# Performance work log

Hardware: AMD Instinct MI355X
Metric: run time of the kernel (lower is better)

The kernel has to match this reference:

```python
import jax, jax.numpy as jnp
import numpy as np

DIM = 512
DIM_HEAD = 32
HEADS = DIM // DIM_HEAD
WS = 8  # window (partition) size
INNER = (DIM * 4 * 2 // 3 // 32) * 32  # gated-MLP inner dim = 2720
EPS = 1e-6
LS_INIT = 1e-5


def _ln(x, g, b):
    mu = jnp.mean(x, axis=-1, keepdims=True)
    var = jnp.var(x, axis=-1, keepdims=True)
    return (x - mu) * jax.lax.rsqrt(var + EPS) * g + b


def setup_inputs() -> dict:
    key = jax.random.key(0)
    ks = jax.random.split(key, 8)
    B, H, W = 8, 96, 96
    s = lambda d: 1.0 / np.sqrt(d)
    return {
        "x": jax.random.normal(ks[0], (B, H, W, DIM), jnp.float32),
        "norm1_g": jnp.ones((DIM,), jnp.float32),
        "norm1_b": jnp.zeros((DIM,), jnp.float32),
        "qkv_w": jax.random.normal(ks[1], (DIM, 3 * DIM), jnp.float32) * s(DIM),
        "qkv_b": jnp.zeros((3 * DIM,), jnp.float32),
        "proj_w": jax.random.normal(ks[2], (DIM, DIM), jnp.float32) * s(DIM),
        "proj_b": jnp.zeros((DIM,), jnp.float32),
        "ls1": jnp.full((DIM,), LS_INIT, jnp.float32),
        "norm2_g": jnp.ones((DIM,), jnp.float32),
        "norm2_b": jnp.zeros((DIM,), jnp.float32),
        "glu_w": jax.random.normal(ks[3], (DIM, 2 * INNER), jnp.float32) * s(DIM),
        "glu_b": jnp.zeros((2 * INNER,), jnp.float32),
        "fc2_w": jax.random.normal(ks[4], (INNER, DIM), jnp.float32) * s(INNER),
        "fc2_b": jnp.zeros((DIM,), jnp.float32),
        "ls2": jnp.full((DIM,), LS_INIT, jnp.float32),
    }


def reference(x, norm1_g, norm1_b, qkv_w, qkv_b, proj_w, proj_b, ls1,
              norm2_g, norm2_b, glu_w, glu_b, fc2_w, fc2_b, ls2):
    B, H, W, C = x.shape
    nH, nW = H // WS, W // WS
    T = WS * WS  # tokens per window

    # ---- window attention branch ----
    y = _ln(x, norm1_g, norm1_b)
    # window_partition: (B,H,W,C) -> (B*nH*nW, T, C)
    y = y.reshape(B, nH, WS, nW, WS, C).transpose(0, 1, 3, 2, 4, 5)
    y = y.reshape(-1, T, C)
    qkv = y @ qkv_w + qkv_b                      # (M, T, 3C)
    qkv = qkv.reshape(-1, T, 3, HEADS, DIM_HEAD)
    q, k, v = qkv[:, :, 0], qkv[:, :, 1], qkv[:, :, 2]   # (M, T, h, d)
    scale = DIM_HEAD ** -0.5
    attn = jnp.einsum('mqhd,mkhd->mhqk', q, k) * scale
    attn = jax.nn.softmax(attn, axis=-1)
    o = jnp.einsum('mhqk,mkhd->mqhd', attn, v).reshape(-1, T, C)
    o = o @ proj_w + proj_b
    # window_reverse: (M, T, C) -> (B, H, W, C)
    o = o.reshape(B, nH, nW, WS, WS, C).transpose(0, 1, 3, 2, 4, 5)
    o = o.reshape(B, H, W, C)
    x = x + ls1 * o

    # ---- gated MLP branch (GLU with SiLU) ----
    y = _ln(x, norm2_g, norm2_b)
    h = y @ glu_w + glu_b
    h, gate = jnp.split(h, 2, axis=-1)
    h = h * jax.nn.silu(gate)
    h = h @ fc2_w + fc2_b
    x = x + ls2 * h
    return x
```

## Files before the change

kernel.cpp:

```cpp
#include <hip/hip_runtime.h>
#include <hip/hip_bf16.h>
#include <stdint.h>

#define DIM 512
#define HEADS 16
#define NTOK 73728
#define INNER 1344
#define INNERP 1408

typedef __attribute__((ext_vector_type(8))) short vbf8;
typedef __attribute__((ext_vector_type(4))) float vf4;
typedef __attribute__((ext_vector_type(4))) int v4i;
typedef __attribute__((ext_vector_type(8))) int v8i;

typedef __attribute__((address_space(1))) void as1void;
typedef __attribute__((address_space(3))) void as3void;

__device__ __forceinline__ unsigned pk4fp8(float a, float b, float c, float d) {
  int v = __builtin_amdgcn_cvt_pk_fp8_f32(a, b, 0, false);
  v = __builtin_amdgcn_cvt_pk_fp8_f32(c, d, v, true);
  return (unsigned)v;
}

__global__ void k_transpose(const float* __restrict__ Wsrc, uint8_t* __restrict__ WT,
                            int K, int N, int ldOut, int nsplit) {
  __shared__ float tile[32][33];
  const int tx = threadIdx.x, ty = threadIdx.y;
  const int n0 = blockIdx.x * 32, k0 = blockIdx.y * 32;
#pragma unroll
  for (int i = 0; i < 32; i += 8) {
    int k = k0 + ty + i, n = n0 + tx;
    if (k < K && n < N) tile[ty + i][tx] = Wsrc[(size_t)k * N + n];
  }
  __syncthreads();
#pragma unroll
  for (int i = 0; i < 32; i += 8) {
    int n = n0 + ty + i, k = k0 + tx;
    if (n < N && k < K) {
      int np = n + (n >= nsplit ? 64 : 0);
      float v = tile[tx][ty + i];
      WT[(size_t)np * ldOut + k] =
          (uint8_t)(__builtin_amdgcn_cvt_pk_fp8_f32(v, v, 0, false) & 0xff);
    }
  }
}

__global__ void k_padbias(const float* __restrict__ b, float* __restrict__ o) {
  int c = blockIdx.x * 256 + threadIdx.x;
  if (c < INNER) o[c] = b[c];
  else if (c >= INNERP && c < INNERP + INNER) o[c] = b[c - 64];
  else if (c < 2816) o[c] = 0.0f;
}

template <bool PART>
__global__ __launch_bounds__(256) void k_ln(const float* __restrict__ x,
                                            const float* __restrict__ gw,
                                            const float* __restrict__ bw,
                                            uint8_t* __restrict__ y) {
  const int wave = threadIdx.x >> 6, lane = threadIdx.x & 63;
  const int tok = blockIdx.x * 4 + wave;
  const float* xr = x + (size_t)tok * DIM + lane * 8;
  const float4 v0 = *(const float4*)xr;
  const float4 v1 = *(const float4*)(xr + 4);
  float s = v0.x + v0.y + v0.z + v0.w + v1.x + v1.y + v1.z + v1.w;
  float ss = v0.x * v0.x + v0.y * v0.y + v0.z * v0.z + v0.w * v0.w +
             v1.x * v1.x + v1.y * v1.y + v1.z * v1.z + v1.w * v1.w;
#pragma unroll
  for (int off = 32; off > 0; off >>= 1) {
    s += __shfl_xor(s, off);
    ss += __shfl_xor(ss, off);
  }
  const float mu = s * (1.0f / DIM);
  const float rs = rsqrtf(ss * (1.0f / DIM) - mu * mu + 1e-6f);
  size_t orow;
  if (PART) {
    int b = tok / 9216, rem = tok % 9216;
    int h = rem / 96, w = rem % 96;
    orow = (size_t)(((b * 12 + (h >> 3)) * 12 + (w >> 3)) * 64 + (h & 7) * 8 + (w & 7));
  } else {
    orow = (size_t)tok;
  }
  const float4 g0 = *(const float4*)(gw + lane * 8);
  const float4 g1 = *(const float4*)(gw + lane * 8 + 4);
  const float4 b0 = *(const float4*)(bw + lane * 8);
  const float4 b1 = *(const float4*)(bw + lane * 8 + 4);
  const float vals[8] = {v0.x, v0.y, v0.z, v0.w, v1.x, v1.y, v1.z, v1.w};
  const float gg[8] = {g0.x, g0.y, g0.z, g0.w, g1.x, g1.y, g1.z, g1.w};
  const float bb[8] = {b0.x, b0.y, b0.z, b0.w, b1.x, b1.y, b1.z, b1.w};
  float r[8];
#pragma unroll
  for (int j = 0; j < 8; ++j) r[j] = (vals[j] - mu) * rs * gg[j] + bb[j];
  uint2 po;
  po.x = pk4fp8(r[0], r[1], r[2], r[3]);
  po.y = pk4fp8(r[4], r[5], r[6], r[7]);
  *(uint2*)(y + orow * DIM + lane * 8) = po;
}

template <int ROWS>
__device__ __forceinline__ void stage_lds8(const uint8_t* __restrict__ g, int ldKb,
                                           char* lds, int wave, int lane) {
  constexpr int RPW = ROWS / 4;
  const int r0 = wave * RPW;
  const int ro = lane >> 3;
  const int pb = lane & 7;
  const uint8_t* src = g + (size_t)(r0 + ro) * (size_t)ldKb + ((pb ^ ro) << 4);
  char* dst = lds + r0 * 128;
#pragma unroll
  for (int c = 0; c < RPW; c += 8) {
    __builtin_amdgcn_global_load_lds((const as1void*)(src + (size_t)c * (size_t)ldKb),
                                     (as3void*)(dst + c * 128), 16, 0, 0);
  }
}

__device__ __forceinline__ v8i lds_frag8(const char* base, int row, int g) {
  const int ro = row & 7;
  const v4i lo = *(const v4i*)(base + row * 128 + (((2 * g) ^ ro) << 4));
  const v4i hi = *(const v4i*)(base + row * 128 + (((2 * g + 1) ^ ro) << 4));
  return __builtin_shufflevector(lo, hi, 0, 1, 2, 3, 4, 5, 6, 7);
}

#define MFMA_SC(a, b, c) \
  __builtin_amdgcn_mfma_scale_f32_16x16x128_f8f6f4((a), (b), (c), 0, 0, 0, 127, 0, 127)

template <int MODE, int NT>
__global__ __launch_bounds__(256, 2) void k_gemm128(const uint8_t* __restrict__ A,
                                                    const uint8_t* __restrict__ BT,
                                                    const float* __restrict__ bias,
                                                    void* __restrict__ outp,
                                                    const float* __restrict__ resid,
                                                    const float* __restrict__ lsv, int K,
                                                    int ldOut) {
  __shared__ alignas(16) char As[128 * 128];
  __shared__ alignas(16) char Bs[128 * 128];
  const int nwg = gridDim.x;
  int bid = blockIdx.x;
  bid = (bid & 7) * (nwg >> 3) + (bid >> 3);
  const int bm = bid / NT, bn = bid % NT;
  const int tid = threadIdx.x;
  const int wave = tid >> 6, lane = tid & 63;
  const int wr = wave >> 1, wc = wave & 1;
  vf4 acc[4][4] = {};

  const uint8_t* Ab = A + (size_t)bm * 128 * K;
  const uint8_t* Bb = BT + (size_t)bn * 128 * K;
  const int cl = lane & 15, g = lane >> 4;
  const int arow = wr * 64 + cl;
  const int brow = wc * 64 + cl;
  const int nkt = K >> 7;

  for (int t = 0; t < nkt; ++t) {
    __syncthreads();
    stage_lds8<128>(Ab + t * 128, K, As, wave, lane);
    stage_lds8<128>(Bb + t * 128, K, Bs, wave, lane);
    __syncthreads();
    v8i af[4], bfr[4];
#pragma unroll
    for (int i = 0; i < 4; ++i) {
      af[i] = lds_frag8(As, arow + i * 16, g);
      bfr[i] = lds_frag8(Bs, brow + i * 16, g);
    }
#pragma unroll
    for (int mi = 0; mi < 4; ++mi)
#pragma unroll
      for (int ni = 0; ni < 4; ++ni)
        acc[mi][ni] = MFMA_SC(af[mi], bfr[ni], acc[mi][ni]);
  }

  const int rl = g << 2;
  const int rbase = bm * 128 + wr * 64;
  const int cbase = bn * 128 + wc * 64;
#pragma unroll
  for (int mi = 0; mi < 4; ++mi) {
#pragma unroll
    for (int j = 0; j < 4; ++j) {
      const int r = rbase + mi * 16 + rl + j;
      size_t orow;
      if (MODE == 1) {
        int m = r >> 6, t = r & 63;
        int b = m / 144, mm = m % 144;
        int wh = mm / 12, ww = mm % 12;
        int h = wh * 8 + (t >> 3), w = ww * 8 + (t & 7);
        orow = (size_t)((b * 96 + h) * 96 + w);
      } else {
        orow = (size_t)r;
      }
#pragma unroll
      for (int ni = 0; ni < 4; ++ni) {
        const int c = cbase + ni * 16 + cl;
        const float v = acc[mi][ni][j] + bias[c];
        if (MODE == 0) {
          ((__hip_bfloat16*)outp)[(size_t)r * ldOut + c] = __float2bfloat16(v);
        } else {
          float* of = (float*)outp;
          of[orow * DIM + c] = resid[orow * DIM + c] + lsv[c] * v;
        }
      }
    }
  }
}

__global__ __launch_bounds__(256, 2) void k_gemm_glu(const uint8_t* __restrict__ A,
                                                     const uint8_t* __restrict__ BT,
                                                     const float* __restrict__ bias,
                                                     uint8_t* __restrict__ hout) {
  __shared__ alignas(16) char As[128 * 128];
  __shared__ alignas(16) char B0s[64 * 128];
  __shared__ alignas(16) char B1s[64 * 128];
  const int K = DIM;
  const int nwg = gridDim.x;
  int bid = blockIdx.x;
  bid = (bid & 7) * (nwg >> 3) + (bid >> 3);
  const int bm = bid / 22, bn = bid % 22;
  const int tid = threadIdx.x;
  const int wave = tid >> 6, lane = tid & 63;
  const int wr = wave >> 1, wc = wave & 1;
  vf4 a0[4][2] = {}, a1[4][2] = {};

  const uint8_t* Ab = A + (size_t)bm * 128 * K;
  const uint8_t* Bb0 = BT + (size_t)(bn * 64) * K;
  const uint8_t* Bb1 = BT + (size_t)(INNERP + bn * 64) * K;
  const int cl = lane & 15, g = lane >> 4;
  const int arow = wr * 64 + cl;
  const int brow = wc * 32 + cl;

#pragma unroll
  for (int t = 0; t < 4; ++t) {
    __syncthreads();
    stage_lds8<128>(Ab + t * 128, K, As, wave, lane);
    stage_lds8<64>(Bb0 + t * 128, K, B0s, wave, lane);
    stage_lds8<64>(Bb1 + t * 128, K, B1s, wave, lane);
    __syncthreads();
    v8i af[4], b0f[2], b1f[2];
#pragma unroll
    for (int i = 0; i < 4; ++i) af[i] = lds_frag8(As, arow + i * 16, g);
#pragma unroll
    for (int i = 0; i < 2; ++i) {
      b0f[i] = lds_frag8(B0s, brow + i * 16, g);
      b1f[i] = lds_frag8(B1s, brow + i * 16, g);
    }
#pragma unroll
    for (int mi = 0; mi < 4; ++mi)
#pragma unroll
      for (int ni = 0; ni < 2; ++ni) {
        a0[mi][ni] = MFMA_SC(af[mi], b0f[ni], a0[mi][ni]);
        a1[mi][ni] = MFMA_SC(af[mi], b1f[ni], a1[mi][ni]);
      }
  }

  const int rl = g << 2;
  const int rbase = bm * 128 + wr * 64;
  const int cbase = bn * 64 + wc * 32;
#pragma unroll
  for (int mi = 0; mi < 4; ++mi)
#pragma unroll
    for (int j = 0; j < 4; ++j) {
      const int r = rbase + mi * 16 + rl + j;
#pragma unroll
      for (int ni = 0; ni < 2; ++ni) {
        const int c = cbase + ni * 16 + cl;
        const float a = a0[mi][ni][j] + bias[c];
        const float gv = a1[mi][ni][j] + bias[INNERP + c];
        const float sg = 1.0f / (1.0f + __expf(-gv));
        const float hv = a * gv * sg;
        hout[(size_t)r * INNERP + c] =
            (uint8_t)(__builtin_amdgcn_cvt_pk_fp8_f32(hv, hv, 0, false) & 0xff);
      }
    }
}

__global__ __launch_bounds__(256, 2) void k_attn_mfma(const __hip_bfloat16* __restrict__ qkv,
                                                      uint8_t* __restrict__ o) {
  __shared__ __hip_bfloat16 sm[4][6912];
  const int wave = threadIdx.x >> 6, lane = threadIdx.x & 63;
  const int task = blockIdx.x * 4 + wave;
  const int w = task >> 4, hd = task & 15;
  const int g = lane >> 4, c = lane & 15;
  __hip_bfloat16* smp = sm[wave];
  __hip_bfloat16* smv = smp + 4608;

  const __hip_bfloat16* base = qkv + (size_t)w * 64 * 1536 + hd * 32;

  vbf8 qf[4], kf[4];
#pragma unroll
  for (int i = 0; i < 4; ++i) {
    const __hip_bfloat16* qrow = base + (size_t)(i * 16 + c) * 1536 + g * 8;
    qf[i] = *(const vbf8*)qrow;
    kf[i] = *(const vbf8*)(qrow + 512);
  }

  {
    const __hip_bfloat16* vrow = base + (size_t)lane * 1536 + 1024;
    union {
      vbf8 v;
      ushort e[8];
    } uv[4];
#pragma unroll
    for (int i = 0; i < 4; ++i) uv[i].v = *(const vbf8*)(vrow + i * 8);
#pragma unroll
    for (int d = 0; d < 32; ++d)
      ((ushort*)smv)[d * 72 + lane] = uv[d >> 3].e[d & 7];
// ... 39 lines not shown
    for (int j = 0; j < 4; ++j) {
      const int q = iq * 16 + g * 4 + j;
#pragma unroll
      for (int it = 0; it < 4; ++it)
        smp[q * 72 + it * 16 + c] = __float2bfloat16(st[iq][it][j]);
    }

  vf4 ot[4][2] = {};
#pragma unroll
  for (int ks = 0; ks < 2; ++ks) {
    vbf8 pf[4], vfr[2];
#pragma unroll
    for (int iq = 0; iq < 4; ++iq)
      pf[iq] = *(const vbf8*)(smp + (iq * 16 + c) * 72 + ks * 32 + g * 8);
#pragma unroll
    for (int dt = 0; dt < 2; ++dt)
      vfr[dt] = *(const vbf8*)(smv + (dt * 16 + c) * 72 + ks * 32 + g * 8);
#pragma unroll
    for (int iq = 0; iq < 4; ++iq)
#pragma unroll
      for (int dt = 0; dt < 2; ++dt)
        ot[iq][dt] = __builtin_amdgcn_mfma_f32_16x16x32_bf16(pf[iq], vfr[dt], ot[iq][dt], 0, 0, 0);
  }

#pragma unroll
  for (int iq = 0; iq < 4; ++iq)
#pragma unroll
    for (int dt = 0; dt < 2; ++dt)
#pragma unroll
      for (int j = 0; j < 4; ++j) {
        const int q = iq * 16 + g * 4 + j;
        smp[q * 72 + dt * 16 + c] = __float2bfloat16(ot[iq][dt][j] * inv[iq][j]);
      }
  uint8_t* ob = o + (size_t)w * 64 * 512 + hd * 32;
#pragma unroll
  for (int i = 0; i < 4; ++i) {
    const int idx = i * 64 + lane;
    const int row = idx >> 2, chunk = idx & 3;
    union {
      vbf8 v;
      ushort e[8];
    } u;
    u.v = *(const vbf8*)(smp + row * 72 + chunk * 8);
    float f[8];
#pragma unroll
    for (int j = 0; j < 8; ++j) f[j] = __uint_as_float((unsigned)u.e[j] << 16);
    uint2 pv;
    pv.x = pk4fp8(f[0], f[1], f[2], f[3]);
    pv.y = pk4fp8(f[4], f[5], f[6], f[7]);
    *(uint2*)(ob + (size_t)row * 512 + chunk * 8) = pv;
  }
}

extern "C" void kernel_launch(void* const* d_in, const int* in_sizes, int n_in, void* d_out,
                              int out_size, void* d_ws, size_t ws_size, hipStream_t stream) {
  const float* x = (const float*)d_in[0];
  const float* n1g = (const float*)d_in[1];
  const float* n1b = (const float*)d_in[2];
  const float* qkv_w = (const float*)d_in[3];
  const float* qkv_b = (const float*)d_in[4];
  const float* proj_w = (const float*)d_in[5];
  const float* proj_b = (const float*)d_in[6];
  const float* ls1 = (const float*)d_in[7];
  const float* n2g = (const float*)d_in[8];
  const float* n2b = (const float*)d_in[9];
  const float* glu_w = (const float*)d_in[10];
  const float* glu_b = (const float*)d_in[11];
  const float* fc2_w = (const float*)d_in[12];
  const float* fc2_b = (const float*)d_in[13];
  const float* ls2 = (const float*)d_in[14];

  if (ws_size < 268000000u) return;

  char* ws = (char*)d_ws;
  uint8_t* wTq = (uint8_t*)(ws + 0);
  uint8_t* wTp = (uint8_t*)(ws + 786432);
  uint8_t* wTg = (uint8_t*)(ws + 1048576);
  uint8_t* wTf = (uint8_t*)(ws + 2490368);
  float* gbias = (float*)(ws + 3211264);
  uint8_t* ybuf = (uint8_t*)(ws + 3222528);
  __hip_bfloat16* qkvbuf = (__hip_bfloat16*)(ws + 40971264);
  uint8_t* hbuf = (uint8_t*)(ws + 40971264);
  float* x1 = (float*)d_out;

  hipMemsetAsync(wTg, 0, 1441792, stream);
  hipMemsetAsync(wTf, 0, 720896, stream);

  dim3 tb(32, 8);
  k_transpose<<<dim3(48, 16), tb, 0, stream>>>(qkv_w, wTq, 512, 1536, 512, 1 << 30);
  k_transpose<<<dim3(16, 16), tb, 0, stream>>>(proj_w, wTp, 512, 512, 512, 1 << 30);
  k_transpose<<<dim3(84, 16), tb, 0, stream>>>(glu_w, wTg, 512, 2688, 512, INNER);
  k_transpose<<<dim3(16, 42), tb, 0, stream>>>(fc2_w, wTf, 1344, 512, 1408, 1 << 30);
  k_padbias<<<11, 256, 0, stream>>>(glu_b, gbias);

  k_ln<true><<<18432, 256, 0, stream>>>(x, n1g, n1b, ybuf);
  k_gemm128<0, 12><<<6912, 256, 0, stream>>>(ybuf, wTq, qkv_b, qkvbuf, nullptr, nullptr, 512, 1536);
  k_attn_mfma<<<4608, 256, 0, stream>>>(qkvbuf, ybuf);
  k_gemm128<1, 4><<<2304, 256, 0, stream>>>(ybuf, wTp, proj_b, (void*)x1, x, ls1, 512, 512);
  k_ln<false><<<18432, 256, 0, stream>>>(x1, n2g, n2b, ybuf);
  k_gemm_glu<<<12672, 256, 0, stream>>>(ybuf, wTg, gbias, hbuf);
  k_gemm128<2, 4><<<2304, 256, 0, stream>>>(hbuf, wTf, fc2_b, d_out, x1, ls2, INNERP, 512);
}
```

Measured before the change: 577.9 us.

## Switch GEMM operands to FP4 with per-32 block weight scales

All activations and weights move from FP8 to FP4 (e2m1). Weights get per-32-element power-of-two block scales, and the GEMMs use the scaled MFMA in fp4 mode with half-size LDS tiles and occupancy raised to 3. The intermediate residual x1 is stored as bf16 instead of fp32, and the GLU epilogue stages results through LDS so it can write packed nibbles. This halves operand bandwidth and LDS traffic, at a large accuracy cost: activations are quantized to FP4 with no scale, which risks exceeding tolerance.

```diff
diff --git a/kernel.cpp b/kernel.cpp
--- a/kernel.cpp
+++ b/kernel.cpp
@@ -1,10 +1,9 @@
 #include <hip/hip_runtime.h>
 #include <hip/hip_bf16.h>
 #include <stdint.h>
+#include <math.h>
 
 #define DIM 512
-#define HEADS 16
-#define NTOK 73728
 #define INNER 1344
 #define INNERP 1408
 
@@ -16,14 +15,31 @@
 typedef __attribute__((address_space(1))) void as1void;
 typedef __attribute__((address_space(3))) void as3void;
 
-__device__ __forceinline__ unsigned pk4fp8(float a, float b, float c, float d) {
-  int v = __builtin_amdgcn_cvt_pk_fp8_f32(a, b, 0, false);
-  v = __builtin_amdgcn_cvt_pk_fp8_f32(c, d, v, true);
-  return (unsigned)v;
-}
-
-__global__ void k_transpose(const float* __restrict__ Wsrc, uint8_t* __restrict__ WT,
-                            int K, int N, int ldOut, int nsplit) {
+union frag8 {
+  v8i w;
+  v4i h[2];
+};
+
+__device__ __forceinline__ uint32_t quant4(float v) {
+  uint32_t s = (__float_as_uint(v) >> 31) << 3;
+  float a = fabsf(v);
+  uint32_t m = (a > 0.25f) + (a > 0.75f) + (a > 1.25f) + (a > 1.75f) +
+               (a > 2.5f) + (a > 3.5f) + (a > 5.0f);
+  return s | m;
+}
+__device__ __forceinline__ uint32_t pack8fp4(const float* r) {
+  uint32_t u = 0;
+#pragma unroll
+  for (int j = 0; j < 8; ++j) u |= quant4(r[j]) << (4 * j);
+  return u;
+}
+
+#define MFMA4(a, b, c, sb) \
+  __builtin_amdgcn_mfma_scale_f32_16x16x128_f8f6f4((a), (b), (c), 4, 4, 0, 127, 0, (sb))
+
+__global__ void k_transpose4(const float* __restrict__ Wsrc, uint8_t* __restrict__ WT,
+                             uint8_t* __restrict__ Wsc, int K, int N, int ldB, int ldS,
+                             int nsplit) {
   __shared__ float tile[32][33];
   const int tx = threadIdx.x, ty = threadIdx.y;
   const int n0 = blockIdx.x * 32, k0 = blockIdx.y * 32;
@@ -33,14 +49,32 @@
     if (k < K && n < N) tile[ty + i][tx] = Wsrc[(size_t)k * N + n];
   }
   __syncthreads();
-#pragma unroll
-  for (int i = 0; i < 32; i += 8) {
-    int n = n0 + ty + i, k = k0 + tx;
-    if (n < N && k < K) {
+  if (tx < 16) {
+#pragma unroll
+    for (int i = 0; i < 32; i += 8) {
+      int n = n0 + ty + i;
+      if (n >= N) continue;
+      float v0 = tile[2 * tx][ty + i], v1 = tile[2 * tx + 1][ty + i];
+      float m = fmaxf(fabsf(v0), fabsf(v1));
+      m = fmaxf(m, __shfl_xor(m, 1));
+      m = fmaxf(m, __shfl_xor(m, 2));
+      m = fmaxf(m, __shfl_xor(m, 4));
+      m = fmaxf(m, __shfl_xor(m, 8));
+      uint8_t sbyte;
+      float s;
+      if (m < 1e-20f) {
+        sbyte = 0;
+        s = 0.0f;
+      } else {
+        int e = (int)ceilf(log2f(m * 0.166666672f));
+        e = e < -126 ? -126 : (e > 126 ? 126 : e);
+        sbyte = (uint8_t)(e + 127);
+        s = exp2f((float)(-e));
+      }
       int np = n + (n >= nsplit ? 64 : 0);
-      float v = tile[tx][ty + i];
-      WT[(size_t)np * ldOut + k] =
-          (uint8_t)(__builtin_amdgcn_cvt_pk_fp8_f32(v, v, 0, false) & 0xff);
+      WT[(size_t)np * ldB + (k0 >> 1) + tx] =
+          (uint8_t)(quant4(v0 * s) | (quant4(v1 * s) << 4));
+      if (tx == 0) Wsc[(size_t)np * ldS + (k0 >> 5)] = sbyte;
     }
   }
 }
@@ -52,19 +86,36 @@
   else if (c < 2816) o[c] = 0.0f;
 }
 
-template <bool PART>
-__global__ __launch_bounds__(256) void k_ln(const float* __restrict__ x,
+template <bool PART, bool BF16IN>
+__global__ __launch_bounds__(256) void k_ln(const void* __restrict__ xin,
                                             const float* __restrict__ gw,
                                             const float* __restrict__ bw,
                                             uint8_t* __restrict__ y) {
   const int wave = threadIdx.x >> 6, lane = threadIdx.x & 63;
   const int tok = blockIdx.x * 4 + wave;
-  const float* xr = x + (size_t)tok * DIM + lane * 8;
-  const float4 v0 = *(const float4*)xr;
-  const float4 v1 = *(const float4*)(xr + 4);
-  float s = v0.x + v0.y + v0.z + v0.w + v1.x + v1.y + v1.z + v1.w;
-  float ss = v0.x * v0.x + v0.y * v0.y + v0.z * v0.z + v0.w * v0.w +
-             v1.x * v1.x + v1.y * v1.y + v1.z * v1.z + v1.w * v1.w;
+  float vals[8];
+  if (BF16IN) {
+    const __hip_bfloat16* xr = (const __hip_bfloat16*)xin + (size_t)tok * DIM + lane * 8;
+    union {
+      vbf8 v;
+      ushort e[8];
+    } u;
+    u.v = *(const vbf8*)xr;
+#pragma unroll
+    for (int j = 0; j < 8; ++j) vals[j] = __uint_as_float((unsigned)u.e[j] << 16);
+  } else {
+    const float* xr = (const float*)xin + (size_t)tok * DIM + lane * 8;
+    const float4 v0 = *(const float4*)xr;
+    const float4 v1 = *(const float4*)(xr + 4);
+    vals[0] = v0.x; vals[1] = v0.y; vals[2] = v0.z; vals[3] = v0.w;
+    vals[4] = v1.x; vals[5] = v1.y; vals[6] = v1.z; vals[7] = v1.w;
+  }
+  float s = 0.f, ss = 0.f;
+#pragma unroll
+  for (int j = 0; j < 8; ++j) {
+    s += vals[j];
+    ss += vals[j] * vals[j];
+  }
 #pragma unroll
   for (int off = 32; off > 0; off >>= 1) {
     s += __shfl_xor(s, off);
@@ -84,86 +135,88 @@
   const float4 g1 = *(const float4*)(gw + lane * 8 + 4);
   const float4 b0 = *(const float4*)(bw + lane * 8);
   const float4 b1 = *(const float4*)(bw + lane * 8 + 4);
-  const float vals[8] = {v0.x, v0.y, v0.z, v0.w, v1.x, v1.y, v1.z, v1.w};
   const float gg[8] = {g0.x, g0.y, g0.z, g0.w, g1.x, g1.y, g1.z, g1.w};
   const float bb[8] = {b0.x, b0.y, b0.z, b0.w, b1.x, b1.y, b1.z, b1.w};
   float r[8];
 #pragma unroll
   for (int j = 0; j < 8; ++j) r[j] = (vals[j] - mu) * rs * gg[j] + bb[j];
-  uint2 po;
-  po.x = pk4fp8(r[0], r[1], r[2], r[3]);
-  po.y = pk4fp8(r[4], r[5], r[6], r[7]);
-  *(uint2*)(y + orow * DIM + lane * 8) = po;
+  *(uint32_t*)(y + orow * 256 + lane * 4) = pack8fp4(r);
 }
 
 template <int ROWS>
-__device__ __forceinline__ void stage_lds8(const uint8_t* __restrict__ g, int ldKb,
-                                           char* lds, int wave, int lane) {
+__device__ __forceinline__ void stage4(const uint8_t* __restrict__ gsrc, int RB, char* lds,
+                                       int wave, int lane) {
   constexpr int RPW = ROWS / 4;
   const int r0 = wave * RPW;
-  const int ro = lane >> 3;
-  const int pb = lane & 7;
-  const uint8_t* src = g + (size_t)(r0 + ro) * (size_t)ldKb + ((pb ^ ro) << 4);
-  char* dst = lds + r0 * 128;
-#pragma unroll
-  for (int c = 0; c < RPW; c += 8) {
-    __builtin_amdgcn_global_load_lds((const as1void*)(src + (size_t)c * (size_t)ldKb),
-                                     (as3void*)(dst + c * 128), 16, 0, 0);
-  }
-}
-
-__device__ __forceinline__ v8i lds_frag8(const char* base, int row, int g) {
-  const int ro = row & 7;
-  const v4i lo = *(const v4i*)(base + row * 128 + (((2 * g) ^ ro) << 4));
-  const v4i hi = *(const v4i*)(base + row * 128 + (((2 * g + 1) ^ ro) << 4));
-  return __builtin_shufflevector(lo, hi, 0, 1, 2, 3, 4, 5, 6, 7);
-}
-
-#define MFMA_SC(a, b, c) \
-  __builtin_amdgcn_mfma_scale_f32_16x16x128_f8f6f4((a), (b), (c), 0, 0, 0, 127, 0, 127)
+  const int srw = lane >> 2, sbk = lane & 3;
+  const uint8_t* src = gsrc + (size_t)(r0 + srw) * RB + ((sbk ^ (srw & 3)) << 4);
+  char* dst = lds + r0 * 64;
+#pragma unroll
+  for (int c = 0; c < RPW; c += 16)
+    __builtin_amdgcn_global_load_lds((const as1void*)(src + (size_t)c * RB),
+                                     (as3void*)(dst + c * 64), 16, 0, 0);
+}
 
 template <int MODE, int NT>
-__global__ __launch_bounds__(256, 2) void k_gemm128(const uint8_t* __restrict__ A,
-                                                    const uint8_t* __restrict__ BT,
-                                                    const float* __restrict__ bias,
-                                                    void* __restrict__ outp,
-                                                    const float* __restrict__ resid,
-                                                    const float* __restrict__ lsv, int K,
-                                                    int ldOut) {
-  __shared__ alignas(16) char As[128 * 128];
-  __shared__ alignas(16) char Bs[128 * 128];
+__global__ __launch_bounds__(256, 3) void k_gemm4(const uint8_t* __restrict__ A4,
+                                                  const uint8_t* __restrict__ B4,
+                                                  const uint8_t* __restrict__ Bsc,
+                                                  const float* __restrict__ bias,
+                                                  void* __restrict__ outp,
+                                                  const void* __restrict__ resid,
+                                                  const float* __restrict__ lsv, const int K,
+                                                  const int ldOut) {
+  __shared__ alignas(16) char As[128 * 64];
+  __shared__ alignas(16) char Bs[128 * 64];
   const int nwg = gridDim.x;
   int bid = blockIdx.x;
   bid = (bid & 7) * (nwg >> 3) + (bid >> 3);
   const int bm = bid / NT, bn = bid % NT;
-  const int tid = threadIdx.x;
-  const int wave = tid >> 6, lane = tid & 63;
+  const int tid = threadIdx.x, wave = tid >> 6, lane = tid & 63;
   const int wr = wave >> 1, wc = wave & 1;
+  const int cl = lane & 15, g = lane >> 4;
+  const int RB = K >> 1, KB = K >> 5, nkt = K >> 7;
+
+  const uint8_t* Ab = A4 + (size_t)bm * 128 * RB;
+  const uint8_t* Bb = B4 + (size_t)bn * 128 * RB;
+
+  int aoff[4], boff[4];
+  const uint8_t* bscp[4];
+#pragma unroll
+  for (int i = 0; i < 4; ++i) {
+    int ra = wr * 64 + cl + i * 16;
+    int rb = wc * 64 + cl + i * 16;
+    aoff[i] = ra * 64 + ((g ^ (ra & 3)) << 4);
+    boff[i] = rb * 64 + ((g ^ (rb & 3)) << 4);
+    bscp[i] = Bsc + (size_t)(bn * 128 + rb) * KB + g;
+  }
+
+  frag8 afr[4], bfr[4];
+#pragma unroll
+  for (int i = 0; i < 4; ++i) {
+    afr[i].w = (v8i){0, 0, 0, 0, 0, 0, 0, 0};
+    bfr[i].w = (v8i){0, 0, 0, 0, 0, 0, 0, 0};
+  }
   vf4 acc[4][4] = {};
-
-  const uint8_t* Ab = A + (size_t)bm * 128 * K;
-  const uint8_t* Bb = BT + (size_t)bn * 128 * K;
-  const int cl = lane & 15, g = lane >> 4;
-  const int arow = wr * 64 + cl;
-  const int brow = wc * 64 + cl;
-  const int nkt = K >> 7;
 
   for (int t = 0; t < nkt; ++t) {
     __syncthreads();
-    stage_lds8<128>(Ab + t * 128, K, As, wave, lane);
-    stage_lds8<128>(Bb + t * 128, K, Bs, wave, lane);
+    stage4<128>(Ab + t * 64, RB, As, wave, lane);
+    stage4<128>(Bb + t * 64, RB, Bs, wave, lane);
     __syncthreads();
-    v8i af[4], bfr[4];
+    int sb[4];
+#pragma unroll
+    for (int i = 0; i < 4; ++i) sb[i] = (int)bscp[i][t * 4];
 #pragma unroll
     for (int i = 0; i < 4; ++i) {
-      af[i] = lds_frag8(As, arow + i * 16, g);
-      bfr[i] = lds_frag8(Bs, brow + i * 16, g);
+      afr[i].h[0] = *(const v4i*)(As + aoff[i]);
+      bfr[i].h[0] = *(const v4i*)(Bs + boff[i]);
     }
 #pragma unroll
     for (int mi = 0; mi < 4; ++mi)
 #pragma unroll
       for (int ni = 0; ni < 4; ++ni)
-        acc[mi][ni] = MFMA_SC(af[mi], bfr[ni], acc[mi][ni]);
+        acc[mi][ni] = MFMA4(afr[mi].w, bfr[ni].w, acc[mi][ni], sb[ni]);
   }
 
   const int rl = g << 2;
@@ -190,82 +243,128 @@
         const float v = acc[mi][ni][j] + bias[c];
         if (MODE == 0) {
           ((__hip_bfloat16*)outp)[(size_t)r * ldOut + c] = __float2bfloat16(v);
+        } else if (MODE == 1) {
+          const float* rx = (const float*)resid;
+          ((__hip_bfloat16*)outp)[orow * DIM + c] =
+              __float2bfloat16(rx[orow * DIM + c] + lsv[c] * v);
         } else {
-          float* of = (float*)outp;
-          of[orow * DIM + c] = resid[orow * DIM + c] + lsv[c] * v;
+          const __hip_bfloat16* rx = (const __hip_bfloat16*)resid;
+          ((float*)outp)[(size_t)r * DIM + c] =
+              __bfloat162float(rx[(size_t)r * DIM + c]) + lsv[c] * v;
         }
       }
     }
   }
 }
 
-__global__ __launch_bounds__(256, 2) void k_gemm_glu(const uint8_t* __restrict__ A,
-                                                     const uint8_t* __restrict__ BT,
-                                                     const float* __restrict__ bias,
-                                                     uint8_t* __restrict__ hout) {
-  __shared__ alignas(16) char As[128 * 128];
-  __shared__ alignas(16) char B0s[64 * 128];
-  __shared__ alignas(16) char B1s[64 * 128];
-  const int K = DIM;
+__global__ __launch_bounds__(256, 3) void k_gemm_glu4(const uint8_t* __restrict__ A4,
+                                                      const uint8_t* __restrict__ B4,
+                                                      const uint8_t* __restrict__ Bsc,
+                                                      const float* __restrict__ bias,
+                                                      uint8_t* __restrict__ hout) {
+  __shared__ alignas(16) char As[128 * 64];
+  __shared__ alignas(16) char B0s[64 * 64];
+  __shared__ alignas(16) char B1s[64 * 64];
+  __shared__ float pane[4][64][17];
+  const int K = DIM, RB = 256, KB = 16;
   const int nwg = gridDim.x;
   int bid = blockIdx.x;
   bid = (bid & 7) * (nwg >> 3) + (bid >> 3);
   const int bm = bid / 22, bn = bid % 22;
-  const int tid = threadIdx.x;
-  const int wave = tid >> 6, lane = tid & 63;
+  const int tid = threadIdx.x, wave = tid >> 6, lane = tid & 63;
   const int wr = wave >> 1, wc = wave & 1;
+  const int cl = lane & 15, g = lane >> 4;
+
+  const uint8_t* Ab = A4 + (size_t)bm * 128 * RB;
+  const uint8_t* Bb0 = B4 + (size_t)(bn * 64) * RB;
+  const uint8_t* Bb1 = B4 + (size_t)(INNERP + bn * 64) * RB;
+
+  int aoff[4], boff[2];
+  const uint8_t* b0scp[2];
+  const uint8_t* b1scp[2];
+#pragma unroll
+  for (int i = 0; i < 4; ++i) {
+    int ra = wr * 64 + cl + i * 16;
+    aoff[i] = ra * 64 + ((g ^ (ra & 3)) << 4);
+  }
+#pragma unroll
+  for (int i = 0; i < 2; ++i) {
+    int rb = wc * 32 + cl + i * 16;
+    boff[i] = rb * 64 + ((g ^ (rb & 3)) << 4);
+    b0scp[i] = Bsc + (size_t)(bn * 64 + rb) * KB + g;
+    b1scp[i] = Bsc + (size_t)(INNERP + bn * 64 + rb) * KB + g;
+  }
+
+  frag8 afr[4], b0f[2], b1f[2];
+#pragma unroll
+  for (int i = 0; i < 4; ++i) afr[i].w = (v8i){0, 0, 0, 0, 0, 0, 0, 0};
+#pragma unroll
+  for (int i = 0; i < 2; ++i) {
+    b0f[i].w = (v8i){0, 0, 0, 0, 0, 0, 0, 0};
+    b1f[i].w = (v8i){0, 0, 0, 0, 0, 0, 0, 0};
+  }
   vf4 a0[4][2] = {}, a1[4][2] = {};
-
-  const uint8_t* Ab = A + (size_t)bm * 128 * K;
-  const uint8_t* Bb0 = BT + (size_t)(bn * 64) * K;
-  const uint8_t* Bb1 = BT + (size_t)(INNERP + bn * 64) * K;
-  const int cl = lane & 15, g = lane >> 4;
-  const int arow = wr * 64 + cl;
-  const int brow = wc * 32 + cl;
 
 #pragma unroll
   for (int t = 0; t < 4; ++t) {
     __syncthreads();
-    stage_lds8<128>(Ab + t * 128, K, As, wave, lane);
-    stage_lds8<64>(Bb0 + t * 128, K, B0s, wave, lane);
-    stage_lds8<64>(Bb1 + t * 128, K, B1s, wave, lane);
+    stage4<128>(Ab + t * 64, RB, As, wave, lane);
+    stage4<64>(Bb0 + t * 64, RB, B0s, wave, lane);
+    stage4<64>(Bb1 + t * 64, RB, B1s, wave, lane);
     __syncthreads();
-    v8i af[4], b0f[2], b1f[2];
-#pragma unroll
-    for (int i = 0; i < 4; ++i) af[i] = lds_frag8(As, arow + i * 16, g);
+    int sb0[2], sb1[2];
 #pragma unroll
     for (int i = 0; i < 2; ++i) {
-      b0f[i] = lds_frag8(B0s, brow + i * 16, g);
-      b1f[i] = lds_frag8(B1s, brow + i * 16, g);
+      sb0[i] = (int)b0scp[i][t * 4];
+      sb1[i] = (int)b1scp[i][t * 4];
+    }
+#pragma unroll
+    for (int i = 0; i < 4; ++i) afr[i].h[0] = *(const v4i*)(As + aoff[i]);
+#pragma unroll
+    for (int i = 0; i < 2; ++i) {
+      b0f[i].h[0] = *(const v4i*)(B0s + boff[i]);
+      b1f[i].h[0] = *(const v4i*)(B1s + boff[i]);
     }
 #pragma unroll
     for (int mi = 0; mi < 4; ++mi)
 #pragma unroll
       for (int ni = 0; ni < 2; ++ni) {
-        a0[mi][ni] = MFMA_SC(af[mi], b0f[ni], a0[mi][ni]);
-        a1[mi][ni] = MFMA_SC(af[mi], b1f[ni], a1[mi][ni]);
-      }
-  }
-
-  const int rl = g << 2;
+        a0[mi][ni] = MFMA4(afr[mi].w, b0f[ni].w, a0[mi][ni], sb0[ni]);
+        a1[mi][ni] = MFMA4(afr[mi].w, b1f[ni].w, a1[mi][ni], sb1[ni]);
+      }
+  }
+
   const int rbase = bm * 128 + wr * 64;
   const int cbase = bn * 64 + wc * 32;
 #pragma unroll
-  for (int mi = 0; mi < 4; ++mi)
-#pragma unroll
-    for (int j = 0; j < 4; ++j) {
-      const int r = rbase + mi * 16 + rl + j;
-#pragma unroll
-      for (int ni = 0; ni < 2; ++ni) {
+  for (int ni = 0; ni < 2; ++ni) {
+#pragma unroll
+    for (int mi = 0; mi < 4; ++mi)
+#pragma unroll
+      for (int j = 0; j < 4; ++j) {
         const int c = cbase + ni * 16 + cl;
         const float a = a0[mi][ni][j] + bias[c];
         const float gv = a1[mi][ni][j] + bias[INNERP + c];
         const float sg = 1.0f / (1.0f + __expf(-gv));
-        const float hv = a * gv * sg;
-        hout[(size_t)r * INNERP + c] =
-            (uint8_t)(__builtin_amdgcn_cvt_pk_fp8_f32(hv, hv, 0, false) & 0xff);
-      }
-    }
+        pane[wave][mi * 16 + g * 4 + j][cl] = a * gv * sg;
+      }
+    asm volatile("s_waitcnt lgkmcnt(0)" ::: "memory");
+    __builtin_amdgcn_sched_barrier(0);
+    {
+      const float* pr = &pane[wave][lane][0];
+      float v0[8], v1[8];
+#pragma unroll
+      for (int b = 0; b < 8; ++b) {
+        v0[b] = pr[b];
+        v1[b] = pr[8 + b];
+      }
+      uint8_t* hp = hout + (size_t)(rbase + lane) * 704 + ((cbase + ni * 16) >> 1);
+      *(uint32_t*)hp = pack8fp4(v0);
+      *(uint32_t*)(hp + 4) = pack8fp4(v1);
+    }
+    asm volatile("s_waitcnt lgkmcnt(0)" ::: "memory");
+    __builtin_amdgcn_sched_barrier(0);
+  }
 }
 
 __global__ __launch_bounds__(256, 2) void k_attn_mfma(const __hip_bfloat16* __restrict__ qkv,
@@ -371,7 +470,7 @@
         const int q = iq * 16 + g * 4 + j;
         smp[q * 72 + dt * 16 + c] = __float2bfloat16(ot[iq][dt][j] * inv[iq][j]);
       }
-  uint8_t* ob = o + (size_t)w * 64 * 512 + hd * 32;
+  uint8_t* ob = o + (size_t)w * 64 * 256 + hd * 16;
 #pragma unroll
   for (int i = 0; i < 4; ++i) {
     const int idx = i * 64 + lane;
@@ -384,10 +483,7 @@
     float f[8];
 #pragma unroll
     for (int j = 0; j < 8; ++j) f[j] = __uint_as_float((unsigned)u.e[j] << 16);
-    uint2 pv;
-    pv.x = pk4fp8(f[0], f[1], f[2], f[3]);
-    pv.y = pk4fp8(f[4], f[5], f[6], f[7]);
-    *(uint2*)(ob + (size_t)row * 512 + chunk * 8) = pv;
+    *(uint32_t*)(ob + (size_t)row * 256 + chunk * 4) = pack8fp4(f);
   }
 }
 
@@ -409,34 +505,41 @@
   const float* fc2_b = (const float*)d_in[13];
   const float* ls2 = (const float*)d_in[14];
 
-  if (ws_size < 268000000u) return;
+  if (ws_size < 248000000u) return;
 
   char* ws = (char*)d_ws;
-  uint8_t* wTq = (uint8_t*)(ws + 0);
-  uint8_t* wTp = (uint8_t*)(ws + 786432);
-  uint8_t* wTg = (uint8_t*)(ws + 1048576);
-  uint8_t* wTf = (uint8_t*)(ws + 2490368);
-  float* gbias = (float*)(ws + 3211264);
-  uint8_t* ybuf = (uint8_t*)(ws + 3222528);
-  __hip_bfloat16* qkvbuf = (__hip_bfloat16*)(ws + 40971264);
-  uint8_t* hbuf = (uint8_t*)(ws + 40971264);
-  float* x1 = (float*)d_out;
-
-  hipMemsetAsync(wTg, 0, 1441792, stream);
-  hipMemsetAsync(wTf, 0, 720896, stream);
+  uint8_t* wTq4 = (uint8_t*)(ws + 0);
+  uint8_t* wTp4 = (uint8_t*)(ws + 393216);
+  uint8_t* wTg4 = (uint8_t*)(ws + 524288);
+  uint8_t* wTf4 = (uint8_t*)(ws + 1245184);
+  uint8_t* sq = (uint8_t*)(ws + 1605632);
+  uint8_t* sp = (uint8_t*)(ws + 1630208);
+  uint8_t* sg = (uint8_t*)(ws + 1638400);
+  uint8_t* sf = (uint8_t*)(ws + 1683456);
+  float* gbias = (float*)(ws + 1705984);
+  uint8_t* act4 = (uint8_t*)(ws + 2097152);
+  char* big = ws + 20971520;
+  __hip_bfloat16* qkvbuf = (__hip_bfloat16*)big;
+  uint8_t* h4 = (uint8_t*)big;
+  __hip_bfloat16* x1b = (__hip_bfloat16*)(big + 69206016);
+
+  hipMemsetAsync(wTg4, 0, 720896, stream);
+  hipMemsetAsync(wTf4, 0, 360448, stream);
+  hipMemsetAsync(sg, 0, 45056, stream);
+  hipMemsetAsync(sf, 0, 22528, stream);
 
   dim3 tb(32, 8);
-  k_transpose<<<dim3(48, 16), tb, 0, stream>>>(qkv_w, wTq, 512, 1536, 512, 1 << 30);
-  k_transpose<<<dim3(16, 16), tb, 0, stream>>>(proj_w, wTp, 512, 512, 512, 1 << 30);
-  k_transpose<<<dim3(84, 16), tb, 0, stream>>>(glu_w, wTg, 512, 2688, 512, INNER);
-  k_transpose<<<dim3(16, 42), tb, 0, stream>>>(fc2_w, wTf, 1344, 512, 1408, 1 << 30);
+  k_transpose4<<<dim3(48, 16), tb, 0, stream>>>(qkv_w, wTq4, sq, 512, 1536, 256, 16, 1 << 30);
+  k_transpose4<<<dim3(16, 16), tb, 0, stream>>>(proj_w, wTp4, sp, 512, 512, 256, 16, 1 << 30);
+  k_transpose4<<<dim3(84, 16), tb, 0, stream>>>(glu_w, wTg4, sg, 512, 2688, 256, 16, INNER);
+  k_transpose4<<<dim3(16, 42), tb, 0, stream>>>(fc2_w, wTf4, sf, 1344, 512, 704, 44, 1 << 30);
   k_padbias<<<11, 256, 0, stream>>>(glu_b, gbias);
 
-  k_ln<true><<<18432, 256, 0, stream>>>(x, n1g, n1b, ybuf);
-  k_gemm128<0, 12><<<6912, 256, 0, stream>>>(ybuf, wTq, qkv_b, qkvbuf, nullptr, nullptr, 512, 1536);
-  k_attn_mfma<<<4608, 256, 0, stream>>>(qkvbuf, ybuf);
-  k_gemm128<1, 4><<<2304, 256, 0, stream>>>(ybuf, wTp, proj_b, (void*)x1, x, ls1, 512, 512);
-  k_ln<false><<<18432, 256, 0, stream>>>(x1, n2g, n2b, ybuf);
-  k_gemm_glu<<<12672, 256, 0, stream>>>(ybuf, wTg, gbias, hbuf);
-  k_gemm128<2, 4><<<2304, 256, 0, stream>>>(hbuf, wTf, fc2_b, d_out, x1, ls2, INNERP, 512);
-}
+  k_ln<true, false><<<18432, 256, 0, stream>>>(x, n1g, n1b, act4);
+  k_gemm4<0, 12><<<6912, 256, 0, stream>>>(act4, wTq4, sq, qkv_b, qkvbuf, nullptr, nullptr, 512, 1536);
+  k_attn_mfma<<<4608, 256, 0, stream>>>(qkvbuf, act4);
+  k_gemm4<1, 4><<<2304, 256, 0, stream>>>(act4, wTp4, sp, proj_b, (void*)x1b, x, ls1, 512, 512);
+  k_ln<false, true><<<18432, 256, 0, stream>>>(x1b, n2g, n2b, act4);
+  k_gemm_glu4<<<12672, 256, 0, stream>>>(act4, wTg4, sg, gbias, h4);
+  k_gemm4<2, 4><<<2304, 256, 0, stream>>>(h4, wTf4, sf, fc2_b, d_out, x1b, ls2, 1408, 512);
+}
```

After: 571.5 us. About the same (-1.1%).

## Store post-attention residual in bf16 and precompute GEMM LDS offsets with constexpr K

Applied to the files above, without the earlier changes.

The intermediate residual x1 is now stored as bf16 in workspace instead of fp32 in the output buffer. LN2 and the fc2 epilogue read it as bf16, which cuts the memory traffic for that stream roughly in half. The GEMM kernels also take K as a template constant, precompute the swizzled LDS fragment offsets outside the k loop, and advance the source pointers incrementally, which reduces per-iteration address arithmetic. Rounding the residual to bf16 adds precision loss to the final output's residual term.

```diff
diff --git a/kernel.cpp b/kernel.cpp
--- a/kernel.cpp
+++ b/kernel.cpp
@@ -3,8 +3,6 @@
 #include <stdint.h>
 
 #define DIM 512
-#define HEADS 16
-#define NTOK 73728
 #define INNER 1344
 #define INNERP 1408
 
@@ -16,11 +14,22 @@
 typedef __attribute__((address_space(1))) void as1void;
 typedef __attribute__((address_space(3))) void as3void;
 
+union frag8 {
+  v8i w;
+  v4i h[2];
+};
+
 __device__ __forceinline__ unsigned pk4fp8(float a, float b, float c, float d) {
   int v = __builtin_amdgcn_cvt_pk_fp8_f32(a, b, 0, false);
   v = __builtin_amdgcn_cvt_pk_fp8_f32(c, d, v, true);
   return (unsigned)v;
 }
+__device__ __forceinline__ uint8_t q8(float v) {
+  return (uint8_t)(__builtin_amdgcn_cvt_pk_fp8_f32(v, v, 0, false) & 0xff);
+}
+
+#define MFMA_SC(a, b, c) \
+  __builtin_amdgcn_mfma_scale_f32_16x16x128_f8f6f4((a), (b), (c), 0, 0, 0, 127, 0, 127)
 
 __global__ void k_transpose(const float* __restrict__ Wsrc, uint8_t* __restrict__ WT,
                             int K, int N, int ldOut, int nsplit) {
@@ -38,9 +47,7 @@
     int n = n0 + ty + i, k = k0 + tx;
     if (n < N && k < K) {
       int np = n + (n >= nsplit ? 64 : 0);
-      float v = tile[tx][ty + i];
-      WT[(size_t)np * ldOut + k] =
-          (uint8_t)(__builtin_amdgcn_cvt_pk_fp8_f32(v, v, 0, false) & 0xff);
+      WT[(size_t)np * ldOut + k] = q8(tile[tx][ty + i]);
     }
   }
 }
@@ -52,19 +59,36 @@
   else if (c < 2816) o[c] = 0.0f;
 }
 
-template <bool PART>
-__global__ __launch_bounds__(256) void k_ln(const float* __restrict__ x,
+template <bool PART, bool BF16IN>
+__global__ __launch_bounds__(256) void k_ln(const void* __restrict__ xin,
                                             const float* __restrict__ gw,
                                             const float* __restrict__ bw,
                                             uint8_t* __restrict__ y) {
   const int wave = threadIdx.x >> 6, lane = threadIdx.x & 63;
   const int tok = blockIdx.x * 4 + wave;
-  const float* xr = x + (size_t)tok * DIM + lane * 8;
-  const float4 v0 = *(const float4*)xr;
-  const float4 v1 = *(const float4*)(xr + 4);
-  float s = v0.x + v0.y + v0.z + v0.w + v1.x + v1.y + v1.z + v1.w;
-  float ss = v0.x * v0.x + v0.y * v0.y + v0.z * v0.z + v0.w * v0.w +
-             v1.x * v1.x + v1.y * v1.y + v1.z * v1.z + v1.w * v1.w;
+  float vals[8];
+  if (BF16IN) {
+    const __hip_bfloat16* xr = (const __hip_bfloat16*)xin + (size_t)tok * DIM + lane * 8;
+    union {
+      vbf8 v;
+      ushort e[8];
+    } u;
+    u.v = *(const vbf8*)xr;
+#pragma unroll
+    for (int j = 0; j < 8; ++j) vals[j] = __uint_as_float((unsigned)u.e[j] << 16);
+  } else {
+    const float* xr = (const float*)xin + (size_t)tok * DIM + lane * 8;
+    const float4 v0 = *(const float4*)xr;
+    const float4 v1 = *(const float4*)(xr + 4);
+    vals[0] = v0.x; vals[1] = v0.y; vals[2] = v0.z; vals[3] = v0.w;
+    vals[4] = v1.x; vals[5] = v1.y; vals[6] = v1.z; vals[7] = v1.w;
+  }
+  float s = 0.f, ss = 0.f;
+#pragma unroll
+  for (int j = 0; j < 8; ++j) {
+    s += vals[j];
+    ss += vals[j] * vals[j];
+  }
 #pragma unroll
   for (int off = 32; off > 0; off >>= 1) {
     s += __shfl_xor(s, off);
@@ -84,7 +108,6 @@
   const float4 g1 = *(const float4*)(gw + lane * 8 + 4);
   const float4 b0 = *(const float4*)(bw + lane * 8);
   const float4 b1 = *(const float4*)(bw + lane * 8 + 4);
-  const float vals[8] = {v0.x, v0.y, v0.z, v0.w, v1.x, v1.y, v1.z, v1.w};
   const float gg[8] = {g0.x, g0.y, g0.z, g0.w, g1.x, g1.y, g1.z, g1.w};
   const float bb[8] = {b0.x, b0.y, b0.z, b0.w, b1.x, b1.y, b1.z, b1.w};
   float r[8];
@@ -96,74 +119,71 @@
   *(uint2*)(y + orow * DIM + lane * 8) = po;
 }
 
-template <int ROWS>
-__device__ __forceinline__ void stage_lds8(const uint8_t* __restrict__ g, int ldKb,
-                                           char* lds, int wave, int lane) {
-  constexpr int RPW = ROWS / 4;
-  const int r0 = wave * RPW;
-  const int ro = lane >> 3;
-  const int pb = lane & 7;
-  const uint8_t* src = g + (size_t)(r0 + ro) * (size_t)ldKb + ((pb ^ ro) << 4);
-  char* dst = lds + r0 * 128;
-#pragma unroll
-  for (int c = 0; c < RPW; c += 8) {
-    __builtin_amdgcn_global_load_lds((const as1void*)(src + (size_t)c * (size_t)ldKb),
-                                     (as3void*)(dst + c * 128), 16, 0, 0);
-  }
-}
-
-__device__ __forceinline__ v8i lds_frag8(const char* base, int row, int g) {
-  const int ro = row & 7;
-  const v4i lo = *(const v4i*)(base + row * 128 + (((2 * g) ^ ro) << 4));
-  const v4i hi = *(const v4i*)(base + row * 128 + (((2 * g + 1) ^ ro) << 4));
-  return __builtin_shufflevector(lo, hi, 0, 1, 2, 3, 4, 5, 6, 7);
-}
-
-#define MFMA_SC(a, b, c) \
-  __builtin_amdgcn_mfma_scale_f32_16x16x128_f8f6f4((a), (b), (c), 0, 0, 0, 127, 0, 127)
-
-template <int MODE, int NT>
-__global__ __launch_bounds__(256, 2) void k_gemm128(const uint8_t* __restrict__ A,
-                                                    const uint8_t* __restrict__ BT,
+template <int K, int MODE, int NT>
+__global__ __launch_bounds__(256, 2) void k_gemm128(const uint8_t* __restrict__ A8,
+                                                    const uint8_t* __restrict__ W8,
                                                     const float* __restrict__ bias,
                                                     void* __restrict__ outp,
-                                                    const float* __restrict__ resid,
-                                                    const float* __restrict__ lsv, int K,
-                                                    int ldOut) {
+                                                    const void* __restrict__ resid,
+                                                    const float* __restrict__ lsv,
+                                                    const int ldOut) {
   __shared__ alignas(16) char As[128 * 128];
-  __shared__ alignas(16) char Bs[128 * 128];
+  __shared__ alignas(16) char Ws[128 * 128];
   const int nwg = gridDim.x;
   int bid = blockIdx.x;
   bid = (bid & 7) * (nwg >> 3) + (bid >> 3);
   const int bm = bid / NT, bn = bid % NT;
-  const int tid = threadIdx.x;
-  const int wave = tid >> 6, lane = tid & 63;
+  const int tid = threadIdx.x, wave = tid >> 6, lane = tid & 63;
   const int wr = wave >> 1, wc = wave & 1;
+  const int cl = lane & 15, g = lane >> 4;
+  constexpr int nkt = K >> 7;
+
+  const int r0 = wave * 32;
+  const int ro = lane >> 3, pb = lane & 7;
+  const int swz = (pb ^ ro) << 4;
+  const uint8_t* asrc = A8 + (size_t)bm * 128 * K + (size_t)(r0 + ro) * K + swz;
+  const uint8_t* wsrc = W8 + (size_t)bn * 128 * K + (size_t)(r0 + ro) * K + swz;
+  char* adst = As + r0 * 128;
+  char* wdst = Ws + r0 * 128;
+
+  int aoff[4][2], woff[4][2];
+#pragma unroll
+  for (int i = 0; i < 4; ++i) {
+    const int ra = wr * 64 + cl + i * 16;
+    const int rb = wc * 64 + cl + i * 16;
+    aoff[i][0] = ra * 128 + (((2 * g) ^ (ra & 7)) << 4);
+    aoff[i][1] = ra * 128 + (((2 * g + 1) ^ (ra & 7)) << 4);
+    woff[i][0] = rb * 128 + (((2 * g) ^ (rb & 7)) << 4);
+    woff[i][1] = rb * 128 + (((2 * g + 1) ^ (rb & 7)) << 4);
+  }
+
   vf4 acc[4][4] = {};
-
-  const uint8_t* Ab = A + (size_t)bm * 128 * K;
-  const uint8_t* Bb = BT + (size_t)bn * 128 * K;
-  const int cl = lane & 15, g = lane >> 4;
-  const int arow = wr * 64 + cl;
-  const int brow = wc * 64 + cl;
-  const int nkt = K >> 7;
 
   for (int t = 0; t < nkt; ++t) {
     __syncthreads();
-    stage_lds8<128>(Ab + t * 128, K, As, wave, lane);
-    stage_lds8<128>(Bb + t * 128, K, Bs, wave, lane);
+#pragma unroll
+    for (int c = 0; c < 32; c += 8) {
+      __builtin_amdgcn_global_load_lds((const as1void*)(asrc + (size_t)c * K),
+                                       (as3void*)(adst + c * 128), 16, 0, 0);
+      __builtin_amdgcn_global_load_lds((const as1void*)(wsrc + (size_t)c * K),
+                                       (as3void*)(wdst + c * 128), 16, 0, 0);
+    }
+    asrc += 128;
+    wsrc += 128;
     __syncthreads();
-    v8i af[4], bfr[4];
+    frag8 af[4], wf[4];
 #pragma unroll
     for (int i = 0; i < 4; ++i) {
-      af[i] = lds_frag8(As, arow + i * 16, g);
-      bfr[i] = lds_frag8(Bs, brow + i * 16, g);
+      af[i].h[0] = *(const v4i*)(As + aoff[i][0]);
+      af[i].h[1] = *(const v4i*)(As + aoff[i][1]);
+      wf[i].h[0] = *(const v4i*)(Ws + woff[i][0]);
+      wf[i].h[1] = *(const v4i*)(Ws + woff[i][1]);
     }
 #pragma unroll
     for (int mi = 0; mi < 4; ++mi)
 #pragma unroll
       for (int ni = 0; ni < 4; ++ni)
-        acc[mi][ni] = MFMA_SC(af[mi], bfr[ni], acc[mi][ni]);
+        acc[mi][ni] = MFMA_SC(af[mi].w, wf[ni].w, acc[mi][ni]);
   }
 
   const int rl = g << 2;
@@ -176,10 +196,10 @@
       const int r = rbase + mi * 16 + rl + j;
       size_t orow;
       if (MODE == 1) {
-        int m = r >> 6, t = r & 63;
+        int m = r >> 6, t2 = r & 63;
         int b = m / 144, mm = m % 144;
         int wh = mm / 12, ww = mm % 12;
-        int h = wh * 8 + (t >> 3), w = ww * 8 + (t & 7);
+        int h = wh * 8 + (t2 >> 3), w = ww * 8 + (t2 & 7);
         orow = (size_t)((b * 96 + h) * 96 + w);
       } else {
         orow = (size_t)r;
@@ -190,60 +210,99 @@
         const float v = acc[mi][ni][j] + bias[c];
         if (MODE == 0) {
           ((__hip_bfloat16*)outp)[(size_t)r * ldOut + c] = __float2bfloat16(v);
+        } else if (MODE == 1) {
+          const float* rx = (const float*)resid;
+          ((__hip_bfloat16*)outp)[orow * DIM + c] =
+              __float2bfloat16(rx[orow * DIM + c] + lsv[c] * v);
         } else {
-          float* of = (float*)outp;
-          of[orow * DIM + c] = resid[orow * DIM + c] + lsv[c] * v;
+          const __hip_bfloat16* rx = (const __hip_bfloat16*)resid;
+          ((float*)outp)[(size_t)r * DIM + c] =
+              __bfloat162float(rx[(size_t)r * DIM + c]) + lsv[c] * v;
         }
       }
     }
   }
 }
 
-__global__ __launch_bounds__(256, 2) void k_gemm_glu(const uint8_t* __restrict__ A,
-                                                     const uint8_t* __restrict__ BT,
+__global__ __launch_bounds__(256, 2) void k_gemm_glu(const uint8_t* __restrict__ A8,
+                                                     const uint8_t* __restrict__ W8,
                                                      const float* __restrict__ bias,
                                                      uint8_t* __restrict__ hout) {
   __shared__ alignas(16) char As[128 * 128];
   __shared__ alignas(16) char B0s[64 * 128];
   __shared__ alignas(16) char B1s[64 * 128];
-  const int K = DIM;
+  constexpr int K = DIM;
   const int nwg = gridDim.x;
   int bid = blockIdx.x;
   bid = (bid & 7) * (nwg >> 3) + (bid >> 3);
   const int bm = bid / 22, bn = bid % 22;
-  const int tid = threadIdx.x;
-  const int wave = tid >> 6, lane = tid & 63;
+  const int tid = threadIdx.x, wave = tid >> 6, lane = tid & 63;
   const int wr = wave >> 1, wc = wave & 1;
+  const int cl = lane & 15, g = lane >> 4;
+
+  const int ro = lane >> 3, pb = lane & 7;
+  const int swz = (pb ^ ro) << 4;
+  const int r0a = wave * 32, r0b = wave * 16;
+  const uint8_t* asrc = A8 + (size_t)bm * 128 * K + (size_t)(r0a + ro) * K + swz;
+  const uint8_t* b0src = W8 + (size_t)(bn * 64 + r0b + ro) * K + swz;
+  const uint8_t* b1src = W8 + (size_t)(INNERP + bn * 64 + r0b + ro) * K + swz;
+  char* adst = As + r0a * 128;
+  char* b0dst = B0s + r0b * 128;
+  char* b1dst = B1s + r0b * 128;
+
+  int aoff[4][2], boff[2][2];
+#pragma unroll
+  for (int i = 0; i < 4; ++i) {
+    const int ra = wr * 64 + cl + i * 16;
+    aoff[i][0] = ra * 128 + (((2 * g) ^ (ra & 7)) << 4);
+    aoff[i][1] = ra * 128 + (((2 * g + 1) ^ (ra & 7)) << 4);
+  }
+#pragma unroll
+  for (int i = 0; i < 2; ++i) {
+    const int rb = wc * 32 + cl + i * 16;
+    boff[i][0] = rb * 128 + (((2 * g) ^ (rb & 7)) << 4);
+    boff[i][1] = rb * 128 + (((2 * g + 1) ^ (rb & 7)) << 4);
+  }
+
   vf4 a0[4][2] = {}, a1[4][2] = {};
-
-  const uint8_t* Ab = A + (size_t)bm * 128 * K;
-  const uint8_t* Bb0 = BT + (size_t)(bn * 64) * K;
-  const uint8_t* Bb1 = BT + (size_t)(INNERP + bn * 64) * K;
-  const int cl = lane & 15, g = lane >> 4;
-  const int arow = wr * 64 + cl;
-  const int brow = wc * 32 + cl;
 
 #pragma unroll
   for (int t = 0; t < 4; ++t) {
     __syncthreads();
-    stage_lds8<128>(Ab + t * 128, K, As, wave, lane);
-    stage_lds8<64>(Bb0 + t * 128, K, B0s, wave, lane);
-    stage_lds8<64>(Bb1 + t * 128, K, B1s, wave, lane);
+#pragma unroll
+    for (int c = 0; c < 32; c += 8)
+      __builtin_amdgcn_global_load_lds((const as1void*)(asrc + (size_t)c * K),
+                                       (as3void*)(adst + c * 128), 16, 0, 0);
+#pragma unroll
+    for (int c = 0; c < 16; c += 8) {
+      __builtin_amdgcn_global_load_lds((const as1void*)(b0src + (size_t)c * K),
+                                       (as3void*)(b0dst + c * 128), 16, 0, 0);
+      __builtin_amdgcn_global_load_lds((const as1void*)(b1src + (size_t)c * K),
+                                       (as3void*)(b1dst + c * 128), 16, 0, 0);
+    }
+    asrc += 128;
+    b0src += 128;
+    b1src += 128;
     __syncthreads();
-    v8i af[4], b0f[2], b1f[2];
-#pragma unroll
-    for (int i = 0; i < 4; ++i) af[i] = lds_frag8(As, arow + i * 16, g);
+    frag8 af[4], w0f[2], w1f[2];
+#pragma unroll
+    for (int i = 0; i < 4; ++i) {
+      af[i].h[0] = *(const v4i*)(As + aoff[i][0]);
+      af[i].h[1] = *(const v4i*)(As + aoff[i][1]);
+    }
 #pragma unroll
     for (int i = 0; i < 2; ++i) {
-      b0f[i] = lds_frag8(B0s, brow + i * 16, g);
-      b1f[i] = lds_frag8(B1s, brow + i * 16, g);
+      w0f[i].h[0] = *(const v4i*)(B0s + boff[i][0]);
+      w0f[i].h[1] = *(const v4i*)(B0s + boff[i][1]);
+      w1f[i].h[0] = *(const v4i*)(B1s + boff[i][0]);
+      w1f[i].h[1] = *(const v4i*)(B1s + boff[i][1]);
     }
 #pragma unroll
     for (int mi = 0; mi < 4; ++mi)
 #pragma unroll
       for (int ni = 0; ni < 2; ++ni) {
-        a0[mi][ni] = MFMA_SC(af[mi], b0f[ni], a0[mi][ni]);
-        a1[mi][ni] = MFMA_SC(af[mi], b1f[ni], a1[mi][ni]);
+        a0[mi][ni] = MFMA_SC(af[mi].w, w0f[ni].w, a0[mi][ni]);
+        a1[mi][ni] = MFMA_SC(af[mi].w, w1f[ni].w, a1[mi][ni]);
       }
   }
 
@@ -261,9 +320,7 @@
         const float a = a0[mi][ni][j] + bias[c];
         const float gv = a1[mi][ni][j] + bias[INNERP + c];
         const float sg = 1.0f / (1.0f + __expf(-gv));
-        const float hv = a * gv * sg;
-        hout[(size_t)r * INNERP + c] =
-            (uint8_t)(__builtin_amdgcn_cvt_pk_fp8_f32(hv, hv, 0, false) & 0xff);
+        hout[(size_t)r * INNERP + c] = q8(a * gv * sg);
       }
     }
 }
@@ -417,10 +474,11 @@
   uint8_t* wTg = (uint8_t*)(ws + 1048576);
   uint8_t* wTf = (uint8_t*)(ws + 2490368);
   float* gbias = (float*)(ws + 3211264);
-  uint8_t* ybuf = (uint8_t*)(ws + 3222528);
-  __hip_bfloat16* qkvbuf = (__hip_bfloat16*)(ws + 40971264);
-  uint8_t* hbuf = (uint8_t*)(ws + 40971264);
-  float* x1 = (float*)d_out;
+  uint8_t* act8 = (uint8_t*)(ws + 3222528);
+  char* big = ws + 40971264;
+  __hip_bfloat16* qkvbuf = (__hip_bfloat16*)big;
+  uint8_t* h8 = (uint8_t*)big;
+  __hip_bfloat16* x1b = (__hip_bfloat16*)(big + 113246208);
 
   hipMemsetAsync(wTg, 0, 1441792, stream);
   hipMemsetAsync(wTf, 0, 720896, stream);
@@ -432,11 +490,11 @@
   k_transpose<<<dim3(16, 42), tb, 0, stream>>>(fc2_w, wTf, 1344, 512, 1408, 1 << 30);
   k_padbias<<<11, 256, 0, stream>>>(glu_b, gbias);
 
-  k_ln<true><<<18432, 256, 0, stream>>>(x, n1g, n1b, ybuf);
-  k_gemm128<0, 12><<<6912, 256, 0, stream>>>(ybuf, wTq, qkv_b, qkvbuf, nullptr, nullptr, 512, 1536);
-  k_attn_mfma<<<4608, 256, 0, stream>>>(qkvbuf, ybuf);
-  k_gemm128<1, 4><<<2304, 256, 0, stream>>>(ybuf, wTp, proj_b, (void*)x1, x, ls1, 512, 512);
-  k_ln<false><<<18432, 256, 0, stream>>>(x1, n2g, n2b, ybuf);
-  k_gemm_glu<<<12672, 256, 0, stream>>>(ybuf, wTg, gbias, hbuf);
-  k_gemm128<2, 4><<<2304, 256, 0, stream>>>(hbuf, wTf, fc2_b, d_out, x1, ls2, INNERP, 512);
-}
+  k_ln<true, false><<<18432, 256, 0, stream>>>(x, n1g, n1b, act8);
+  k_gemm128<512, 0, 12><<<6912, 256, 0, stream>>>(act8, wTq, qkv_b, qkvbuf, nullptr, nullptr, 1536);
+  k_attn_mfma<<<4608, 256, 0, stream>>>(qkvbuf, act8);
+  k_gemm128<512, 1, 4><<<2304, 256, 0, stream>>>(act8, wTp, proj_b, (void*)x1b, x, ls1, 512);
+  k_ln<false, true><<<18432, 256, 0, stream>>>(x1b, n2g, n2b, act8);
+  k_gemm_glu<<<12672, 256, 0, stream>>>(act8, wTg, gbias, h8);
+  k_gemm128<1408, 2, 4><<<2304, 256, 0, stream>>>(h8, wTf, fc2_b, d_out, x1b, ls2, 512);
+}
```

New measurement: 552.3 us. 1.05x faster.
